# Optimization experiments

Measured on AMD Instinct MI355X. Metric: run time of the kernel, lower is better.

## Reference

```python
import jax, jax.numpy as jnp
import numpy as np

B, S, H = 16, 512, 768
T, HD = 9, 64  # num_entity_types, head_size
MASK_VAL = 1e12


def setup_inputs() -> dict:
    key = jax.random.key(0)
    k1, k2 = jax.random.split(key)
    hidden_states = jax.random.normal(k1, (B, S, H), dtype=jnp.float32)
    attention_mask = jnp.ones((B, S), dtype=jnp.int32)
    W_dense = jax.random.normal(k2, (H, T * HD * 2), dtype=jnp.float32) * (H ** -0.5)
    b_dense = jnp.zeros((T * HD * 2,), dtype=jnp.float32)
    return {"hidden_states": hidden_states, "attention_mask": attention_mask,
            "W_dense": W_dense, "b_dense": b_dense}


def _rope_rotate(x, cos_pos, sin_pos):
    # x: [B, S, T, HD]; rotate interleaved pairs
    x2 = jnp.stack([-x[..., 1::2], x[..., ::2]], axis=-1).reshape(x.shape)
    return x * cos_pos + x2 * sin_pos


def reference(hidden_states, attention_mask, W_dense, b_dense):
    b, s, _ = hidden_states.shape
    out = hidden_states @ W_dense + b_dense              # [B,S,T*HD*2]
    out = out.reshape(b, s, T, HD, 2)
    qw, kw = out[..., 0], out[..., 1]                    # [B,S,T,HD]

    # sinusoidal RoPE angles
    pos = jnp.arange(s, dtype=jnp.float32)               # [S]
    inv_freq = jnp.power(10000.0, -2.0 * jnp.arange(HD // 2, dtype=jnp.float32) / HD)
    ang = pos[:, None] * inv_freq[None, :]               # [S, HD/2]
    cos_pos = jnp.repeat(jnp.cos(ang), 2, axis=-1)[None, :, None, :]  # [1,S,1,HD]
    sin_pos = jnp.repeat(jnp.sin(ang), 2, axis=-1)[None, :, None, :]

    qw = _rope_rotate(qw, cos_pos, sin_pos)
    kw = _rope_rotate(kw, cos_pos, sin_pos)

    # biaffine scores: [B,T,S,S]
    logits = jnp.einsum('bmtd,bntd->btmn', qw, kw) / (HD ** 0.5)

    am = attention_mask.astype(logits.dtype)
    pad_mask = (am[:, :, None] * am[:, None, :])[:, None, :, :]  # [B,1,S,S]
    logits = logits - (1.0 - pad_mask) * MASK_VAL

    triu = jnp.triu(jnp.ones((s, s), dtype=logits.dtype), k=0)
    logits = logits - (1.0 - triu) * MASK_VAL
    return logits
```

## Files before the change

### kernel.cpp

```cpp
#include <hip/hip_runtime.h>

#define B_  16
#define S_  512
#define H_  768
#define T_  9
#define HD_ 64
#define N1  (T_*HD_*2)
#define M1  (B_*S_)
#define NT1 (H_/32)

typedef __attribute__((ext_vector_type(8))) short bf16x8;
typedef __attribute__((ext_vector_type(4))) float f32x4;

#define GLB(p) ((const __attribute__((address_space(1))) void*)(p))
#define LDSP(p) ((__attribute__((address_space(3))) void*)(p))

__device__ inline unsigned short f2bf(float f){
  union { float f; unsigned u; } v; v.f = f;
  unsigned r = v.u + 0x7fffu + ((v.u >> 16) & 1u);
  return (unsigned short)(r >> 16);
}

__global__ __launch_bounds__(256) void prep_wt(
    const float* __restrict__ W, short* __restrict__ Wt, float2* __restrict__ tab)
{
  __shared__ float tile[32][33];
  const int bx = blockIdx.x, tid = threadIdx.x;
  if(bx < 864){
    int n0 = (bx % 36)*32, k0 = (bx / 36)*32;
    int tx = tid & 31, ty = tid >> 5;
    #pragma unroll
    for(int r = 0; r < 32; r += 8)
      tile[ty + r][tx] = W[(size_t)(k0 + ty + r)*N1 + n0 + tx];
    __syncthreads();
    #pragma unroll
    for(int r = 0; r < 32; r += 8)
      Wt[(size_t)(n0 + ty + r)*H_ + k0 + tx] = (short)f2bf(tile[tx][ty + r]);
  } else {
    int i = (bx - 864)*256 + tid;
    int s = i >> 5, p = i & 31;
    float inv = powf(10000.f, -2.f*(float)p/64.f);
    float a = (float)s * inv;
    tab[i] = make_float2(cosf(a), sinf(a));
  }
}

__global__ __launch_bounds__(256, 4) void gemm1_rope(
    const float* __restrict__ hs, const short* __restrict__ Wt,
    const float* __restrict__ bias, const float2* __restrict__ tab,
    short* __restrict__ Qr, short* __restrict__ Kr)
{
  __shared__ short As[2][64*32];
  __shared__ short Bs[2][128*32];
  const int tid  = threadIdx.x;
  const int lane = tid & 63, w = tid >> 6;
  const int wm = (w & 1) * 32, wn = (w >> 1) * 64;
  const int m0 = blockIdx.x * 64, n0 = blockIdx.y * 128;
  const int lr = lane & 15, lk = (lane >> 4) * 8;

  const int ar = tid >> 2, ac = (tid & 3) * 8;
  const float* aS = hs + (size_t)(m0 + ar) * H_ + ac;
  const short* bS = Wt + (size_t)(n0 + ar) * H_ + ac;
  const int dOff = tid * 8;

  f32x4 acc[2][4] = {};
  float4 ra0, ra1;

#define CVT_DSWRITE(buf) do{ \
    bf16x8 t_; \
    t_[0]=f2bf(ra0.x); t_[1]=f2bf(ra0.y); t_[2]=f2bf(ra0.z); t_[3]=f2bf(ra0.w); \
    t_[4]=f2bf(ra1.x); t_[5]=f2bf(ra1.y); t_[6]=f2bf(ra1.z); t_[7]=f2bf(ra1.w); \
    *(bf16x8*)(&As[buf][dOff]) = t_; \
  }while(0)

#define STAGE_B(buf, k0) do{ \
    __builtin_amdgcn_global_load_lds(GLB(bS + (k0)),          LDSP(&Bs[buf][dOff]),        16, 0, 0); \
    __builtin_amdgcn_global_load_lds(GLB(bS + 64*H_ + (k0)),  LDSP(&Bs[buf][2048 + dOff]), 16, 0, 0); \
  }while(0)

  ra0 = *(const float4*)(aS);  ra1 = *(const float4*)(aS + 4);
  CVT_DSWRITE(0);
  STAGE_B(0, 0);
  __builtin_amdgcn_sched_barrier(0);
  ra0 = *(const float4*)(aS + 32);  ra1 = *(const float4*)(aS + 36);
  __builtin_amdgcn_sched_barrier(0);
  asm volatile("s_waitcnt vmcnt(2)" ::: "memory");
  asm volatile("s_waitcnt lgkmcnt(0)" ::: "memory");
  __builtin_amdgcn_s_barrier();

  for(int k = 0; k < NT1; ++k){
    const int cur = k & 1, nxt = cur ^ 1;
    if(k + 1 < NT1){
      CVT_DSWRITE(nxt);
      STAGE_B(nxt, (k + 1) * 32);
    }
    __builtin_amdgcn_sched_barrier(0);
    if(k + 2 < NT1){
      ra0 = *(const float4*)(aS + (k + 2) * 32);
      ra1 = *(const float4*)(aS + (k + 2) * 32 + 4);
    }
    __builtin_amdgcn_sched_barrier(0);

    bf16x8 aF[2], bF[4];
    #pragma unroll
    for(int i = 0; i < 2; ++i) aF[i] = *(const bf16x8*)(&As[cur][(wm + i*16 + lr)*32 + lk]);
    #pragma unroll
    for(int j = 0; j < 4; ++j) bF[j] = *(const bf16x8*)(&Bs[cur][(wn + j*16 + lr)*32 + lk]);
    #pragma unroll
    for(int i = 0; i < 2; ++i)
      #pragma unroll
      for(int j = 0; j < 4; ++j)
        acc[i][j] = __builtin_amdgcn_mfma_f32_16x16x32_bf16(bF[j], aF[i], acc[i][j], 0, 0, 0);

    if(k + 1 < NT1){
      if(k + 2 < NT1) asm volatile("s_waitcnt vmcnt(2)" ::: "memory");
      else            asm volatile("s_waitcnt vmcnt(0)" ::: "memory");
      asm volatile("s_waitcnt lgkmcnt(0)" ::: "memory");
      __builtin_amdgcn_s_barrier();
    }
  }

  const int t = n0 >> 7;
  #pragma unroll
  for(int i = 0; i < 2; ++i){
    int m  = m0 + wm + i*16 + lr;
    int bi = m >> 9, sp = m & 511;
    size_t rowoff = ((size_t)(bi*T_ + t)*S_ + sp)*HD_;
    #pragma unroll
    for(int j = 0; j < 4; ++j){
      int nq  = n0 + wn + j*16 + ((lane >> 4) << 2);
      int hd0 = (nq >> 1) & 63;
      int p   = (nq >> 2) & 31;
      float4 bv = *(const float4*)(bias + nq);
      float2 cs = tab[sp*32 + p];
      float q0 = acc[i][j][0] + bv.x;
      float k0v= acc[i][j][1] + bv.y;
      float q1 = acc[i][j][2] + bv.z;
      float k1v= acc[i][j][3] + bv.w;
      float rq0 = q0*cs.x - q1*cs.y, rq1 = q1*cs.x + q0*cs.y;
      float rk0 = k0v*cs.x - k1v*cs.y, rk1 = k1v*cs.x + k0v*cs.y;
      unsigned uq = (unsigned)f2bf(rq0) | ((unsigned)f2bf(rq1) << 16);
      unsigned uk = (unsigned)f2bf(rk0) | ((unsigned)f2bf(rk1) << 16);
      *(unsigned*)(Qr + rowoff + hd0) = uq;
      *(unsigned*)(Kr + rowoff + hd0) = uk;
    }
  }
#undef CVT_DSWRITE
#undef STAGE_B
}

__global__ __launch_bounds__(256) void gemm2_mask(
    const short* __restrict__ Qr, const short* __restrict__ Kr,
    const int* __restrict__ am, float* __restrict__ out)
{
  const int lane = threadIdx.x & 63;
  const int w    = threadIdx.x >> 6;
  const int bt   = blockIdx.z;
  const int b    = bt / T_;
  const int n0   = blockIdx.x * 128 + (w & 1) * 64;
  const int m0   = blockIdx.y * 128 + (w >> 1) * 64;
  const int lr   = lane & 15;
  const int lk   = (lane >> 4) * 8;

  const short* Q = Qr + (size_t)bt * S_ * HD_;
  const short* K = Kr + (size_t)bt * S_ * HD_;
  f32x4 acc[4][4] = {};

  #pragma unroll
  for(int ks = 0; ks < HD_; ks += 32){
    bf16x8 aF[4], bF[4];
    #pragma unroll
    for(int i = 0; i < 4; ++i) aF[i] = *(const bf16x8*)(Q + (size_t)(m0 + i*16 + lr)*HD_ + ks + lk);
    #pragma unroll
    for(int j = 0; j < 4; ++j) bF[j] = *(const bf16x8*)(K + (size_t)(n0 + j*16 + lr)*HD_ + ks + lk);
    #pragma unroll
    for(int i = 0; i < 4; ++i)
      #pragma unroll
      for(int j = 0; j < 4; ++j)
        acc[i][j] = __builtin_amdgcn_mfma_f32_16x16x32_bf16(bF[j], aF[i], acc[i][j], 0, 0, 0);
  }

  const int* amb = am + b * S_;
  #pragma unroll
  for(int i = 0; i < 4; ++i){
    int m = m0 + i*16 + lr;
    float amm = (float)amb[m];
    float* orow = out + ((size_t)bt*S_ + m)*S_;
    #pragma unroll
    for(int j = 0; j < 4; ++j){
      int nq = n0 + j*16 + ((lane >> 4) << 2);
      int4 a4 = *(const int4*)(amb + nq);
      float4 r;
      r.x = acc[i][j][0]*0.125f - (1.f - amm*(float)a4.x)*1e12f - ((nq+0) < m ? 1e12f : 0.f);
      r.y = acc[i][j][1]*0.125f - (1.f - amm*(float)a4.y)*1e12f - ((nq+1) < m ? 1e12f : 0.f);
      r.z = acc[i][j][2]*0.125f - (1.f - amm*(float)a4.z)*1e12f - ((nq+2) < m ? 1e12f : 0.f);
      r.w = acc[i][j][3]*0.125f - (1.f - amm*(float)a4.w)*1e12f - ((nq+3) < m ? 1e12f : 0.f);
      *(float4*)(orow + nq) = r;
    }
  }
}

extern "C" void kernel_launch(void* const* d_in, const int* in_sizes, int n_in,
                              void* d_out, int out_size, void* d_ws, size_t ws_size,
                              hipStream_t stream)
{
  const float* hs    = (const float*)d_in[0];
  const int*   amask = (const int*)  d_in[1];
  const float* W     = (const float*)d_in[2];
  const float* bias  = (const float*)d_in[3];
  float* out = (float*)d_out;

  char* ws = (char*)d_ws;
  short*  Wt  = (short*) (ws);
  float2* tab = (float2*)(ws + 1769472);
  short*  Qr  = (short*) (ws + 1900544);
  short*  Kr  = (short*) (ws + 11337728);

  prep_wt  <<<928, 256, 0, stream>>>(W, Wt, tab);
  gemm1_rope<<<dim3(M1/64, N1/128), 256, 0, stream>>>(hs, Wt, bias, tab, Qr, Kr);
  gemm2_mask<<<dim3(S_/128, S_/128, B_*T_), 256, 0, stream>>>(Qr, Kr, amask, out);
}
```

Baseline: 94.42 us.

## Shrink gemm1 tile to 64x64, reorder grid, simplify sync to __syncthreads

The QK projection GEMM tile shrinks from 64x128 to 64x64, which doubles the block count and halves per-thread accumulators. The launch-bounds occupancy hint rises from 4 to 6, and the grid is transposed so N blocks vary fastest, keeping nearby blocks on the same A rows. The hand-written vmcnt/lgkmcnt waits and sched barriers are replaced with a plain __syncthreads at the top of each k-step. That may drain the in-flight A prefetch each iteration and lose some load/compute overlap, and the smaller tile also cuts data reuse per block.

```diff
diff --git a/kernel.cpp b/kernel.cpp
--- a/kernel.cpp
+++ b/kernel.cpp
@@ -45,79 +45,63 @@
   }
 }
 
-__global__ __launch_bounds__(256, 4) void gemm1_rope(
+__global__ __launch_bounds__(256, 6) void gemm1_rope(
     const float* __restrict__ hs, const short* __restrict__ Wt,
     const float* __restrict__ bias, const float2* __restrict__ tab,
     short* __restrict__ Qr, short* __restrict__ Kr)
 {
   __shared__ short As[2][64*32];
-  __shared__ short Bs[2][128*32];
+  __shared__ short Bs[2][64*32];
   const int tid  = threadIdx.x;
   const int lane = tid & 63, w = tid >> 6;
-  const int wm = (w & 1) * 32, wn = (w >> 1) * 64;
-  const int m0 = blockIdx.x * 64, n0 = blockIdx.y * 128;
-  const int lr = lane & 15, lk = (lane >> 4) * 8;
-
-  const int ar = tid >> 2, ac = (tid & 3) * 8;
-  const float* aS = hs + (size_t)(m0 + ar) * H_ + ac;
-  const short* bS = Wt + (size_t)(n0 + ar) * H_ + ac;
+  const int lr = lane & 15, h = lane >> 4;
+  const int lk = h * 8;
+  const int wm = (w & 1) * 32, wn = (w >> 1) * 32;
+  const int n0 = blockIdx.x * 64;
+  const int m0 = blockIdx.y * 64;
+
+  const float* aS = hs + (size_t)(m0 + (tid >> 2)) * H_ + (tid & 3) * 8;
+  const short* bS = Wt + (size_t)(n0 + (tid >> 2)) * H_ + (tid & 3) * 8;
   const int dOff = tid * 8;
 
-  f32x4 acc[2][4] = {};
+  f32x4 acc[2][2] = {};
   float4 ra0, ra1;
 
+#define LOAD_A(k0) do{ ra0 = *(const float4*)(aS + (k0)); \
+                       ra1 = *(const float4*)(aS + (k0) + 4); }while(0)
 #define CVT_DSWRITE(buf) do{ \
     bf16x8 t_; \
     t_[0]=f2bf(ra0.x); t_[1]=f2bf(ra0.y); t_[2]=f2bf(ra0.z); t_[3]=f2bf(ra0.w); \
     t_[4]=f2bf(ra1.x); t_[5]=f2bf(ra1.y); t_[6]=f2bf(ra1.z); t_[7]=f2bf(ra1.w); \
     *(bf16x8*)(&As[buf][dOff]) = t_; \
   }while(0)
-
-#define STAGE_B(buf, k0) do{ \
-    __builtin_amdgcn_global_load_lds(GLB(bS + (k0)),          LDSP(&Bs[buf][dOff]),        16, 0, 0); \
-    __builtin_amdgcn_global_load_lds(GLB(bS + 64*H_ + (k0)),  LDSP(&Bs[buf][2048 + dOff]), 16, 0, 0); \
-  }while(0)
-
-  ra0 = *(const float4*)(aS);  ra1 = *(const float4*)(aS + 4);
+#define STAGE_B(buf, k0) \
+    __builtin_amdgcn_global_load_lds(GLB(bS + (k0)), LDSP(&Bs[buf][dOff]), 16, 0, 0)
+
+  LOAD_A(0);
   CVT_DSWRITE(0);
   STAGE_B(0, 0);
-  __builtin_amdgcn_sched_barrier(0);
-  ra0 = *(const float4*)(aS + 32);  ra1 = *(const float4*)(aS + 36);
-  __builtin_amdgcn_sched_barrier(0);
-  asm volatile("s_waitcnt vmcnt(2)" ::: "memory");
-  asm volatile("s_waitcnt lgkmcnt(0)" ::: "memory");
-  __builtin_amdgcn_s_barrier();
+  LOAD_A(32);
 
   for(int k = 0; k < NT1; ++k){
-    const int cur = k & 1, nxt = cur ^ 1;
+    __syncthreads();
+    const int cur = k & 1;
     if(k + 1 < NT1){
-      CVT_DSWRITE(nxt);
-      STAGE_B(nxt, (k + 1) * 32);
+      CVT_DSWRITE(cur ^ 1);
+      STAGE_B(cur ^ 1, (k + 1) * 32);
     }
-    __builtin_amdgcn_sched_barrier(0);
-    if(k + 2 < NT1){
-      ra0 = *(const float4*)(aS + (k + 2) * 32);
-      ra1 = *(const float4*)(aS + (k + 2) * 32 + 4);
-    }
-    __builtin_amdgcn_sched_barrier(0);
-
-    bf16x8 aF[2], bF[4];
+    if(k + 2 < NT1) LOAD_A((k + 2) * 32);
+
+    bf16x8 aF[2], bF[2];
     #pragma unroll
     for(int i = 0; i < 2; ++i) aF[i] = *(const bf16x8*)(&As[cur][(wm + i*16 + lr)*32 + lk]);
     #pragma unroll
-    for(int j = 0; j < 4; ++j) bF[j] = *(const bf16x8*)(&Bs[cur][(wn + j*16 + lr)*32 + lk]);
+    for(int j = 0; j < 2; ++j) bF[j] = *(const bf16x8*)(&Bs[cur][(wn + j*16 + lr)*32 + lk]);
     #pragma unroll
     for(int i = 0; i < 2; ++i)
       #pragma unroll
-      for(int j = 0; j < 4; ++j)
+      for(int j = 0; j < 2; ++j)
         acc[i][j] = __builtin_amdgcn_mfma_f32_16x16x32_bf16(bF[j], aF[i], acc[i][j], 0, 0, 0);
-
-    if(k + 1 < NT1){
-      if(k + 2 < NT1) asm volatile("s_waitcnt vmcnt(2)" ::: "memory");
-      else            asm volatile("s_waitcnt vmcnt(0)" ::: "memory");
-      asm volatile("s_waitcnt lgkmcnt(0)" ::: "memory");
-      __builtin_amdgcn_s_barrier();
-    }
   }
 
   const int t = n0 >> 7;
@@ -127,8 +111,8 @@
     int bi = m >> 9, sp = m & 511;
     size_t rowoff = ((size_t)(bi*T_ + t)*S_ + sp)*HD_;
     #pragma unroll
-    for(int j = 0; j < 4; ++j){
-      int nq  = n0 + wn + j*16 + ((lane >> 4) << 2);
+    for(int j = 0; j < 2; ++j){
+      int nq  = n0 + wn + j*16 + (h << 2);
       int hd0 = (nq >> 1) & 63;
       int p   = (nq >> 2) & 31;
       float4 bv = *(const float4*)(bias + nq);
@@ -145,6 +129,7 @@
       *(unsigned*)(Kr + rowoff + hd0) = uk;
     }
   }
+#undef LOAD_A
 #undef CVT_DSWRITE
 #undef STAGE_B
 }
@@ -216,7 +201,7 @@
   short*  Qr  = (short*) (ws + 1900544);
   short*  Kr  = (short*) (ws + 11337728);
 
-  prep_wt  <<<928, 256, 0, stream>>>(W, Wt, tab);
-  gemm1_rope<<<dim3(M1/64, N1/128), 256, 0, stream>>>(hs, Wt, bias, tab, Qr, Kr);
+  prep_wt   <<<928, 256, 0, stream>>>(W, Wt, tab);
+  gemm1_rope<<<dim3(N1/64, M1/64), 256, 0, stream>>>(hs, Wt, bias, tab, Qr, Kr);
   gemm2_mask<<<dim3(S_/128, S_/128, B_*T_), 256, 0, stream>>>(Qr, Kr, amask, out);
 }
```

Measured after the change: 108.2 us. +14.6%, slower.
